# Kernel optimization log

Hardware: AMD Instinct MI355X
Metric: run time of the kernel (lower is better)

The kernel has to match this reference:

```python
import jax, jax.numpy as jnp
import numpy as np

N = 20000
IN_CH = 256
HID = 32
HEADS = 8
OUT_CH = 40
NEG_SLOPE = 0.2


def _gat_layer(x, src, dst, W, a_src, a_dst, b, heads, ch, concat):
    # x: [N, F_in], W: [F_in, heads*ch], a_src/a_dst: [heads, ch], b: [heads*ch] or [ch]
    n = x.shape[0]
    h = (x @ W).reshape(n, heads, ch)                      # [N, H, C]
    alpha_s = jnp.einsum('nhc,hc->nh', h, a_src)           # [N, H]
    alpha_d = jnp.einsum('nhc,hc->nh', h, a_dst)           # [N, H]
    e = jax.nn.leaky_relu(alpha_s[src] + alpha_d[dst], NEG_SLOPE)  # [E, H]
    # segment softmax over edges sharing the same destination node
    m = jax.ops.segment_max(e, dst, num_segments=n)        # [N, H]
    ex = jnp.exp(e - m[dst])                               # [E, H]
    denom = jax.ops.segment_sum(ex, dst, num_segments=n)   # [N, H]
    alpha = ex / (denom[dst] + 1e-16)                      # [E, H]
    out = jax.ops.segment_sum(h[src] * alpha[:, :, None], dst, num_segments=n)  # [N, H, C]
    out = out.reshape(n, heads * ch) if concat else out.mean(axis=1)
    return out + b


def setup_inputs() -> dict:
    key = jax.random.key(0)
    ks = jax.random.split(key, 12)
    x = jax.random.normal(ks[0], (N, IN_CH), dtype=jnp.float32)
    edge_index = jax.random.randint(ks[1], (2, 320000), 0, N, dtype=jnp.int64)
    s1 = 1.0 / np.sqrt(IN_CH)
    s2 = 1.0 / np.sqrt(HEADS * HID)
    W1 = jax.random.uniform(ks[2], (IN_CH, HEADS * HID), jnp.float32, -s1, s1)
    a1_src = jax.random.uniform(ks[3], (HEADS, HID), jnp.float32, -s2, s2)
    a1_dst = jax.random.uniform(ks[4], (HEADS, HID), jnp.float32, -s2, s2)
    b1 = jnp.zeros((HEADS * HID,), jnp.float32)
    W2 = jax.random.uniform(ks[5], (HEADS * HID, OUT_CH), jnp.float32, -s2, s2)
    so = 1.0 / np.sqrt(OUT_CH)
    a2_src = jax.random.uniform(ks[6], (1, OUT_CH), jnp.float32, -so, so)
    a2_dst = jax.random.uniform(ks[7], (1, OUT_CH), jnp.float32, -so, so)
    b2 = jnp.zeros((OUT_CH,), jnp.float32)
    return {"x": x, "edge_index": edge_index, "W1": W1, "a1_src": a1_src,
            "a1_dst": a1_dst, "b1": b1, "W2": W2, "a2_src": a2_src,
            "a2_dst": a2_dst, "b2": b2}


def reference(x, edge_index, W1, a1_src, a1_dst, b1, W2, a2_src, a2_dst, b2):
    n = x.shape[0]
    loop = jnp.arange(n, dtype=edge_index.dtype)
    src = jnp.concatenate([edge_index[0], loop])  # PyG adds self-loops by default
    dst = jnp.concatenate([edge_index[1], loop])
    # dropout layers are identity in eval mode
    h = _gat_layer(x, src, dst, W1, a1_src, a1_dst, b1, HEADS, HID, concat=True)
    h = jax.nn.elu(h)
    out = _gat_layer(h, src, dst, W2, a2_src, a2_dst, b2, 1, OUT_CH, concat=False)
    return jax.nn.log_softmax(out, axis=1)
```

## Files before the change

kernel.cpp:

```cpp
#include <hip/hip_runtime.h>
#include <math.h>

#define N_NODES 20000
#define E_RAW   320000
#define E_TOT   (E_RAW + N_NODES)
#define IN_CH   256
#define HEADS   8
#define HID     32
#define HH      (HEADS*HID)
#define OUT_CH  40
#define NC2     48
#define NEG     0.2f

typedef __attribute__((ext_vector_type(8))) short  short8;
typedef __attribute__((ext_vector_type(4))) float  floatx4;

__device__ __forceinline__ unsigned short f2bf(float f) {
    unsigned int u = __float_as_uint(f);
    unsigned int r = (u + 0x7FFFu + ((u >> 16) & 1u)) >> 16;
    return (unsigned short)r;
}
__device__ __forceinline__ float bf2f(unsigned short h) {
    return __uint_as_float(((unsigned int)h) << 16);
}
__device__ __forceinline__ float lexp(float v) {
    v = (v > 0.f) ? v : NEG * v;
    return __expf(v);
}


__global__ void setup_kernel(const float* __restrict__ W1,
                             const float* __restrict__ W2,
                             unsigned short* __restrict__ w1t,
                             unsigned short* __restrict__ w2t,
                             int* __restrict__ deg) {
    int b = blockIdx.x;
    int t = threadIdx.x;
    if (b < 79) {
        int i = b * 256 + t;
        if (i < N_NODES) deg[i] = 0;
    } else if (b < 79 + HH) {
        int c = b - 79;
        w1t[c * IN_CH + t] = f2bf(W1[(size_t)t * HH + c]);
    } else {
        int c = b - 79 - HH;
        w2t[c * HH + t] = (c < OUT_CH) ? f2bf(W2[(size_t)t * OUT_CH + c]) : 0;
    }
}


__global__ void hist_kernel(const int* __restrict__ ei, int* __restrict__ deg,
                            int* __restrict__ pos) {
    int e = blockIdx.x * 256 + threadIdx.x;
    if (e >= E_TOT) return;
    int d = (e < E_RAW) ? ei[E_RAW + e] : (e - E_RAW);
    pos[e] = atomicAdd(&deg[d], 1);
}

__global__ __launch_bounds__(1024) void scan_kernel(const int* __restrict__ deg,
                                                    int* __restrict__ offs) {
    __shared__ int part[1024];
    int t = threadIdx.x;
    const int chunk = 20;
    int begin = t * chunk;
    bool in = (begin < N_NODES);
    int loc[20];
    if (in) {
        #pragma unroll
        for (int v4 = 0; v4 < 5; v4++) {
            int4 v = *reinterpret_cast<const int4*>(&deg[begin + v4 * 4]);
            loc[v4*4+0] = v.x; loc[v4*4+1] = v.y; loc[v4*4+2] = v.z; loc[v4*4+3] = v.w;
        }
    } else {
        #pragma unroll
        for (int i = 0; i < 20; i++) loc[i] = 0;
    }
    int s = 0;
    #pragma unroll
    for (int i = 0; i < 20; i++) s += loc[i];
    part[t] = s;
    __syncthreads();
    for (int off = 1; off < 1024; off <<= 1) {
        int v = (t >= off) ? part[t - off] : 0;
        __syncthreads();
        part[t] += v;
        __syncthreads();
    }
    int run = (t == 0) ? 0 : part[t - 1];
    if (in) {
        #pragma unroll
        for (int i = 0; i < 20; i++) { offs[begin + i] = run; run += loc[i]; }
    }
    if (t == 1023) offs[N_NODES] = part[1023];
}

__global__ void scatter_kernel(const int* __restrict__ ei, const int* __restrict__ offs,
                               const int* __restrict__ pos, int* __restrict__ csr) {
    int e = blockIdx.x * 256 + threadIdx.x;
    if (e >= E_TOT) return;
    int s, d;
    if (e < E_RAW) { s = ei[e]; d = ei[E_RAW + e]; }
    else           { s = e - E_RAW; d = s; }
    csr[offs[d] + pos[e]] = s;
}

#define G1_LDK 72
__global__ __launch_bounds__(256) void gemm1(const float* __restrict__ x,
                                             const unsigned short* __restrict__ w1t,
                                             const float* __restrict__ a1s,
                                             const float* __restrict__ a1d,
                                             unsigned short* __restrict__ h1b,
                                             float* __restrict__ as1,
                                             float* __restrict__ ad1) {
    __shared__ unsigned short As[64 * G1_LDK];
    __shared__ unsigned short Bs[128 * G1_LDK];
    int t = threadIdx.x;
    int wave = t >> 6, lane = t & 63;
    int ln = lane & 15, q = lane >> 4;
    int bm = blockIdx.x >> 1;
    int bn = blockIdx.x & 1;
    int n0 = bm * 64;
    int c0 = bn * 128;

    floatx4 acc[8];
    #pragma unroll
    for (int f = 0; f < 8; f++) acc[f] = (floatx4){0.f, 0.f, 0.f, 0.f};

    int srow = t >> 4, scol = t & 15;

    for (int kc = 0; kc < IN_CH; kc += 64) {
        #pragma unroll
        for (int pp = 0; pp < 4; pp++) {
            int row = srow + pp * 16;
            int n = n0 + row;
            float4 v = (n < N_NODES)
                ? *reinterpret_cast<const float4*>(&x[(size_t)n * IN_CH + kc + scol * 4])
                : make_float4(0.f, 0.f, 0.f, 0.f);
            ushort4 pv;
            pv.x = f2bf(v.x); pv.y = f2bf(v.y); pv.z = f2bf(v.z); pv.w = f2bf(v.w);
            *reinterpret_cast<ushort4*>(&As[row * G1_LDK + scol * 4]) = pv;
        }
        #pragma unroll
        for (int pp = 0; pp < 8; pp++) {
            int row = srow + pp * 16;
            *reinterpret_cast<ushort4*>(&Bs[row * G1_LDK + scol * 4]) =
                *reinterpret_cast<const ushort4*>(&w1t[(size_t)(c0 + row) * IN_CH + kc + scol * 4]);
        }
        __syncthreads();
        #pragma unroll
        for (int ks = 0; ks < 2; ks++) {
            short8 a = *reinterpret_cast<const short8*>(
                &As[(16 * wave + ln) * G1_LDK + ks * 32 + q * 8]);
            #pragma unroll
            for (int f = 0; f < 8; f++) {
                short8 b = *reinterpret_cast<const short8*>(
                    &Bs[(16 * f + ln) * G1_LDK + ks * 32 + q * 8]);
                acc[f] = __builtin_amdgcn_mfma_f32_16x16x32_bf16(a, b, acc[f], 0, 0, 0);
            }
        }
        __syncthreads();
    }

    float Asr[8], Adr[8];
    #pragma unroll
    for (int f = 0; f < 8; f++) {
        Asr[f] = a1s[c0 + 16 * f + ln];
        Adr[f] = a1d[c0 + 16 * f + ln];
    }
    #pragma unroll
    for (int f = 0; f < 8; f++) {
        #pragma unroll
        for (int r = 0; r < 4; r++) {
            int n = n0 + 16 * wave + q * 4 + r;
            if (n < N_NODES)
                h1b[(size_t)n * HH + c0 + 16 * f + ln] = f2bf(acc[f][r]);
        }
    }
    int h0 = c0 >> 5;
    #pragma unroll
    for (int lh = 0; lh < 4; lh++) {
        #pragma unroll
        for (int r = 0; r < 4; r++) {
            float ps = acc[2*lh][r] * Asr[2*lh] + acc[2*lh+1][r] * Asr[2*lh+1];
            float pd = acc[2*lh][r] * Adr[2*lh] + acc[2*lh+1][r] * Adr[2*lh+1];
            ps += __shfl_xor(ps, 1); ps += __shfl_xor(ps, 2);
            ps += __shfl_xor(ps, 4); ps += __shfl_xor(ps, 8);
            pd += __shfl_xor(pd, 1); pd += __shfl_xor(pd, 2);
            pd += __shfl_xor(pd, 4); pd += __shfl_xor(pd, 8);
            int n = n0 + 16 * wave + q * 4 + r;
            if (ln == 0 && n < N_NODES) {
                as1[n * HEADS + h0 + lh] = ps;
                ad1[n * HEADS + h0 + lh] = pd;
            }
        }
    }
}


__global__ __launch_bounds__(256) void aggr1(const unsigned short* __restrict__ h1b,
                                             const float* __restrict__ as1,
                                             const float* __restrict__ ad1,
                                             const float* __restrict__ b1,
                                             const int* __restrict__ offs,
                                             const int* __restrict__ csr,
                                             unsigned short* __restrict__ h2b) {
    int d = blockIdx.x * 4 + (threadIdx.x >> 6);
    int lane = threadIdx.x & 63;
    int h = lane >> 3;
    int c4 = lane * 4;
    int start = offs[d];
    int deg = offs[d + 1] - start;
    float adv = ad1[d * HEADS + h];

    float a0 = 0.f, a1 = 0.f, a2 = 0.f, a3 = 0.f, den = 0.f;
    int jj = 0;
    for (; jj + 8 <= deg; jj += 8) {
        int s[8];
        #pragma unroll
        for (int i = 0; i < 8; i++) s[i] = csr[start + jj + i];
        float e[8];
        #pragma unroll
        for (int i = 0; i < 8; i++) e[i] = as1[s[i] * HEADS + h];
        ushort4 pv[8];
        #pragma unroll
        for (int i = 0; i < 8; i++)
            pv[i] = *reinterpret_cast<const ushort4*>(&h1b[(size_t)s[i] * HH + c4]);
        #pragma unroll
        for (int i = 0; i < 8; i++) {
            float w = lexp(e[i] + adv);
            den += w;
            a0 = fmaf(bf2f(pv[i].x), w, a0);
            a1 = fmaf(bf2f(pv[i].y), w, a1);
            a2 = fmaf(bf2f(pv[i].z), w, a2);
            a3 = fmaf(bf2f(pv[i].w), w, a3);
        }
    }
    for (; jj < deg; jj++) {
        int s = csr[start + jj];
        float w = lexp(as1[s * HEADS + h] + adv);
        den += w;
        ushort4 pv = *reinterpret_cast<const ushort4*>(&h1b[(size_t)s * HH + c4]);
        a0 = fmaf(bf2f(pv.x), w, a0);
        a1 = fmaf(bf2f(pv.y), w, a1);
        a2 = fmaf(bf2f(pv.z), w, a2);
        a3 = fmaf(bf2f(pv.w), w, a3);
    }
    float inv = 1.0f / (den + 1e-16f);
    float4 bv = *reinterpret_cast<const float4*>(&b1[c4]);
    float r0 = a0 * inv + bv.x;
    float r1 = a1 * inv + bv.y;
    float r2 = a2 * inv + bv.z;
    float r3 = a3 * inv + bv.w;
    r0 = (r0 > 0.f) ? r0 : (__expf(r0) - 1.f);
    r1 = (r1 > 0.f) ? r1 : (__expf(r1) - 1.f);
    r2 = (r2 > 0.f) ? r2 : (__expf(r2) - 1.f);
    r3 = (r3 > 0.f) ? r3 : (__expf(r3) - 1.f);
    ushort4 ov;
    ov.x = f2bf(r0); ov.y = f2bf(r1); ov.z = f2bf(r2); ov.w = f2bf(r3);
    *reinterpret_cast<ushort4*>(&h2b[(size_t)d * HH + c4]) = ov;
}

#define G2_LDK 264
__global__ __launch_bounds__(256) void gemm2(const unsigned short* __restrict__ h2b,
                                             const unsigned short* __restrict__ w2t,
                                             const float* __restrict__ a2s,
                                             const float* __restrict__ a2d,
                                             unsigned short* __restrict__ h3b,
                                             float* __restrict__ as2,
                                             float* __restrict__ ad2) {
    __shared__ unsigned short As2[64 * G2_LDK];
    __shared__ unsigned short Bs2[NC2 * G2_LDK];
    int t = threadIdx.x;
    int wave = t >> 6, lane = t & 63;
    int ln = lane & 15, q = lane >> 4;
    int n0 = blockIdx.x * 64;

    {
        int row = t >> 2, seg = t & 3;
        int n = n0 + row;
        #pragma unroll
        for (int i = 0; i < 8; i++) {
            short8 v;
            if (n < N_NODES)
                v = *reinterpret_cast<const short8*>(&h2b[(size_t)n * HH + seg * 64 + i * 8]);
            else
                v = (short8){0,0,0,0,0,0,0,0};
            *reinterpret_cast<short8*>(&As2[row * G2_LDK + seg * 64 + i * 8]) = v;
        }
    }
    for (int u = t; u < NC2 * 32; u += 256) {
        int row = u >> 5;
        int col = (u & 31) * 8;
        *reinterpret_cast<short8*>(&Bs2[row * G2_LDK + col]) =
            *reinterpret_cast<const short8*>(&w2t[(size_t)row * HH + col]);
    }
    __syncthreads();

    floatx4 acc[3];
    #pragma unroll
    for (int f = 0; f < 3; f++) acc[f] = (floatx4){0.f, 0.f, 0.f, 0.f};

    #pragma unroll
    for (int kf = 0; kf < 8; kf++) {
        short8 a = *reinterpret_cast<const short8*>(
            &As2[(16 * wave + ln) * G2_LDK + kf * 32 + q * 8]);
        #pragma unroll
        for (int f = 0; f < 3; f++) {
            short8 b = *reinterpret_cast<const short8*>(
                &Bs2[(16 * f + ln) * G2_LDK + kf * 32 + q * 8]);
            acc[f] = __builtin_amdgcn_mfma_f32_16x16x32_bf16(a, b, acc[f], 0, 0, 0);
        }
    }

    float a2sv[3], a2dv[3];
    #pragma unroll
    for (int f = 0; f < 3; f++) {
        int c = 16 * f + ln;
        a2sv[f] = (c < OUT_CH) ? a2s[c] : 0.f;
        a2dv[f] = (c < OUT_CH) ? a2d[c] : 0.f;
    }
    #pragma unroll
    for (int r = 0; r < 4; r++) {
        int n = n0 + 16 * wave + q * 4 + r;
        float ps = acc[0][r] * a2sv[0] + acc[1][r] * a2sv[1] + acc[2][r] * a2sv[2];
        float pd = acc[0][r] * a2dv[0] + acc[1][r] * a2dv[1] + acc[2][r] * a2dv[2];
        ps += __shfl_xor(ps, 1); ps += __shfl_xor(ps, 2);
        ps += __shfl_xor(ps, 4); ps += __shfl_xor(ps, 8);
        pd += __shfl_xor(pd, 1); pd += __shfl_xor(pd, 2);
        pd += __shfl_xor(pd, 4); pd += __shfl_xor(pd, 8);
        if (n < N_NODES) {
            #pragma unroll
            for (int f = 0; f < 3; f++) {
                int c = 16 * f + ln;
                if (c < OUT_CH)
                    h3b[(size_t)n * OUT_CH + c] = f2bf(acc[f][r]);
            }
            if (ln == 0) { as2[n] = ps; ad2[n] = pd; }
        }
    }
}


__global__ __launch_bounds__(256) void aggr2(const unsigned short* __restrict__ h3b,
                                             const float* __restrict__ as2,
                                             const float* __restrict__ ad2,
                                             const float* __restrict__ b2,
                                             const int* __restrict__ offs,
                                             const int* __restrict__ csr,
                                             float* __restrict__ out) {
    int d = blockIdx.x * 4 + (threadIdx.x >> 6);
    int lane = threadIdx.x & 63;
    int start = offs[d];
    int deg = offs[d + 1] - start;
    float adv = ad2[d];
    bool ok = (lane < OUT_CH);
    int cl = ok ? lane : 0;

    float acc = 0.f, den = 0.f;
    int jj = 0;
    for (; jj + 8 <= deg; jj += 8) {
        int s[8];
        #pragma unroll
        for (int i = 0; i < 8; i++) s[i] = csr[start + jj + i];
        float e[8];
        #pragma unroll
        for (int i = 0; i < 8; i++) e[i] = as2[s[i]];
        unsigned short qv[8];
        #pragma unroll
        for (int i = 0; i < 8; i++) qv[i] = h3b[(size_t)s[i] * OUT_CH + cl];
        #pragma unroll
        for (int i = 0; i < 8; i++) {
            float w = lexp(e[i] + adv);
            den += w;
            acc = fmaf(bf2f(qv[i]), w, acc);
        }
    }
    for (; jj < deg; jj++) {
        int s = csr[start + jj];
        float w = lexp(as2[s] + adv);
        den += w;
        acc = fmaf(bf2f(h3b[(size_t)s * OUT_CH + cl]), w, acc);
    }

    float r = ok ? (acc / (den + 1e-16f) + b2[lane]) : -1e30f;
    float mx = r;
    #pragma unroll
    for (int off = 32; off >= 1; off >>= 1) mx = fmaxf(mx, __shfl_xor(mx, off));
    float ex = ok ? __expf(r - mx) : 0.f;
    float se = ex;
    #pragma unroll
    for (int off = 32; off >= 1; off >>= 1) se += __shfl_xor(se, off);
    if (ok) out[(size_t)d * OUT_CH + lane] = r - mx - __logf(se);
}


extern "C" void kernel_launch(void* const* d_in, const int* in_sizes, int n_in,
                              void* d_out, int out_size, void* d_ws, size_t ws_size,
                              hipStream_t stream) {
    const float* x   = (const float*)d_in[0];
    const int*   ei  = (const int*)  d_in[1];
    const float* W1  = (const float*)d_in[2];
    const float* a1s = (const float*)d_in[3];
    const float* a1d = (const float*)d_in[4];
    const float* b1  = (const float*)d_in[5];
    const float* W2  = (const float*)d_in[6];
    const float* a2s = (const float*)d_in[7];
    const float* a2d = (const float*)d_in[8];
    const float* b2  = (const float*)d_in[9];
    float* out = (float*)d_out;

    char* p = (char*)d_ws;
    auto alloc = [&](size_t bytes) {
        char* r = p;
        p += (bytes + 255) & ~(size_t)255;
        return r;
    };
    unsigned short* h1b = (unsigned short*)alloc((size_t)N_NODES * HH * 2);
    unsigned short* h2b = (unsigned short*)alloc((size_t)N_NODES * HH * 2);
    unsigned short* h3b = (unsigned short*)alloc((size_t)N_NODES * OUT_CH * 2);
    unsigned short* w1t = (unsigned short*)alloc((size_t)IN_CH * HH * 2);
    unsigned short* w2t = (unsigned short*)alloc((size_t)NC2 * HH * 2);
    float* as1  = (float*)alloc((size_t)N_NODES * HEADS * 4);
    float* ad1  = (float*)alloc((size_t)N_NODES * HEADS * 4);
    float* as2v = (float*)alloc((size_t)N_NODES * 4);
    float* ad2v = (float*)alloc((size_t)N_NODES * 4);
    int* deg    = (int*)alloc((size_t)N_NODES * 4);
    int* pos    = (int*)alloc((size_t)E_TOT * 4);
    int* offs   = (int*)alloc((size_t)(N_NODES + 1) * 4);
    int* csr    = (int*)alloc((size_t)E_TOT * 4);

    setup_kernel<<<79 + HH + NC2, 256, 0, stream>>>(W1, W2, w1t, w2t, deg);
    hist_kernel<<<(E_TOT + 255) / 256, 256, 0, stream>>>(ei, deg, pos);
    scan_kernel<<<1, 1024, 0, stream>>>(deg, offs);
    scatter_kernel<<<(E_TOT + 255) / 256, 256, 0, stream>>>(ei, offs, pos, csr);

    gemm1<<<313 * 2, 256, 0, stream>>>(x, w1t, a1s, a1d, h1b, as1, ad1);
    aggr1<<<N_NODES / 4, 256, 0, stream>>>(h1b, as1, ad1, b1, offs, csr, h2b);
    gemm2<<<313, 256, 0, stream>>>(h2b, w2t, a2s, a2d, h3b, as2v, ad2v);
    aggr2<<<N_NODES / 4, 256, 0, stream>>>(h3b, as2v, ad2v, b2, offs, csr, out);
}
```

Before: 179.9 us.

## Fuse histogram into setup, scatter into gemm1, use wave-shuffle scan

```diff
diff --git a/kernel.cpp b/kernel.cpp
--- a/kernel.cpp
+++ b/kernel.cpp
@@ -12,6 +12,9 @@
 #define NC2     48
 #define NEG     0.2f
 
+#define HIST_BLKS ((E_TOT + 255) / 256)
+#define G1_BLKS   313
+
 typedef __attribute__((ext_vector_type(8))) short  short8;
 typedef __attribute__((ext_vector_type(4))) float  floatx4;
 
@@ -29,38 +32,35 @@
 }
 
 
-__global__ void setup_kernel(const float* __restrict__ W1,
-                             const float* __restrict__ W2,
-                             unsigned short* __restrict__ w1t,
-                             unsigned short* __restrict__ w2t,
-                             int* __restrict__ deg) {
+__global__ void setup_hist(const int* __restrict__ ei,
+                           const float* __restrict__ W1,
+                           const float* __restrict__ W2,
+                           unsigned short* __restrict__ w1t,
+                           unsigned short* __restrict__ w2t,
+                           int* __restrict__ deg,
+                           int* __restrict__ pos) {
     int b = blockIdx.x;
     int t = threadIdx.x;
-    if (b < 79) {
-        int i = b * 256 + t;
-        if (i < N_NODES) deg[i] = 0;
-    } else if (b < 79 + HH) {
-        int c = b - 79;
+    if (b < HIST_BLKS) {
+        int e = b * 256 + t;
+        if (e >= E_TOT) return;
+        int d = (e < E_RAW) ? ei[E_RAW + e] : (e - E_RAW);
+        pos[e] = atomicAdd(&deg[d], 1);
+    } else if (b < HIST_BLKS + HH) {
+        int c = b - HIST_BLKS;
         w1t[c * IN_CH + t] = f2bf(W1[(size_t)t * HH + c]);
     } else {
-        int c = b - 79 - HH;
-        w2t[c * HH + t] = (c < OUT_CH) ? f2bf(W2[(size_t)t * OUT_CH + c]) : 0;
-    }
-}
-
-
-__global__ void hist_kernel(const int* __restrict__ ei, int* __restrict__ deg,
-                            int* __restrict__ pos) {
-    int e = blockIdx.x * 256 + threadIdx.x;
-    if (e >= E_TOT) return;
-    int d = (e < E_RAW) ? ei[E_RAW + e] : (e - E_RAW);
-    pos[e] = atomicAdd(&deg[d], 1);
-}
+        int c = b - HIST_BLKS - HH;
+        w2t[c * HH + t] = (c < OUT_CH) ? f2bf(W2[(size_t)t * OUT_CH + c]) : (unsigned short)0;
+    }
+}
+
 
 __global__ __launch_bounds__(1024) void scan_kernel(const int* __restrict__ deg,
                                                     int* __restrict__ offs) {
-    __shared__ int part[1024];
+    __shared__ int wsum[16], wpre[16];
     int t = threadIdx.x;
+    int lane = t & 63, wave = t >> 6;
     const int chunk = 20;
     int begin = t * chunk;
     bool in = (begin < N_NODES);
@@ -78,30 +78,38 @@
     int s = 0;
     #pragma unroll
     for (int i = 0; i < 20; i++) s += loc[i];
-    part[t] = s;
+    int sc = s;
+    #pragma unroll
+    for (int off = 1; off < 64; off <<= 1) {
+        int v = __shfl_up(sc, off);
+        if (lane >= off) sc += v;
+    }
+    if (lane == 63) wsum[wave] = sc;
     __syncthreads();
-    for (int off = 1; off < 1024; off <<= 1) {
-        int v = (t >= off) ? part[t - off] : 0;
-        __syncthreads();
-        part[t] += v;
-        __syncthreads();
-    }
-    int run = (t == 0) ? 0 : part[t - 1];
+    if (t < 16) {
+        int v = wsum[t];
+        int p = v;
+        #pragma unroll
+        for (int off = 1; off < 16; off <<= 1) {
+            int u = __shfl_up(p, off);
+            if (t >= off) p += u;
+        }
+        wpre[t] = p - v;
+    }
+    __syncthreads();
+    int run = wpre[wave] + sc - s;
     if (in) {
         #pragma unroll
-        for (int i = 0; i < 20; i++) { offs[begin + i] = run; run += loc[i]; }
-    }
-    if (t == 1023) offs[N_NODES] = part[1023];
-}
-
-__global__ void scatter_kernel(const int* __restrict__ ei, const int* __restrict__ offs,
-                               const int* __restrict__ pos, int* __restrict__ csr) {
-    int e = blockIdx.x * 256 + threadIdx.x;
-    if (e >= E_TOT) return;
-    int s, d;
-    if (e < E_RAW) { s = ei[e]; d = ei[E_RAW + e]; }
-    else           { s = e - E_RAW; d = s; }
-    csr[offs[d] + pos[e]] = s;
+        for (int v4 = 0; v4 < 5; v4++) {
+            int4 o;
+            o.x = run; run += loc[v4*4+0];
+            o.y = run; run += loc[v4*4+1];
+            o.z = run; run += loc[v4*4+2];
+            o.w = run; run += loc[v4*4+3];
+            *reinterpret_cast<int4*>(&offs[begin + v4 * 4]) = o;
+        }
+    }
+    if (t == 0) offs[N_NODES] = E_TOT;
 }
 
 #define G1_LDK 72
@@ -111,20 +119,33 @@
                                              const float* __restrict__ a1d,
                                              unsigned short* __restrict__ h1b,
                                              float* __restrict__ as1,
-                                             float* __restrict__ ad1) {
+                                             float* __restrict__ ad1,
+                                             const int* __restrict__ ei,
+                                             const int* __restrict__ offs,
+                                             const int* __restrict__ pos,
+                                             int* __restrict__ csr) {
     __shared__ unsigned short As[64 * G1_LDK];
-    __shared__ unsigned short Bs[128 * G1_LDK];
+    __shared__ unsigned short Bs[256 * G1_LDK];
     int t = threadIdx.x;
+
+    if (blockIdx.x >= G1_BLKS) {
+        int e = (blockIdx.x - G1_BLKS) * 256 + t;
+        if (e < E_TOT) {
+            int s, d;
+            if (e < E_RAW) { s = ei[e]; d = ei[E_RAW + e]; }
+            else           { s = e - E_RAW; d = s; }
+            csr[offs[d] + pos[e]] = s;
+        }
+        return;
+    }
+
     int wave = t >> 6, lane = t & 63;
     int ln = lane & 15, q = lane >> 4;
-    int bm = blockIdx.x >> 1;
-    int bn = blockIdx.x & 1;
-    int n0 = bm * 64;
-    int c0 = bn * 128;
-
-    floatx4 acc[8];
-    #pragma unroll
-    for (int f = 0; f < 8; f++) acc[f] = (floatx4){0.f, 0.f, 0.f, 0.f};
+    int n0 = blockIdx.x * 64;
+
+    floatx4 acc[16];
+    #pragma unroll
+    for (int f = 0; f < 16; f++) acc[f] = (floatx4){0.f, 0.f, 0.f, 0.f};
 
     int srow = t >> 4, scol = t & 15;
 
@@ -141,10 +162,10 @@
             *reinterpret_cast<ushort4*>(&As[row * G1_LDK + scol * 4]) = pv;
         }
         #pragma unroll
-        for (int pp = 0; pp < 8; pp++) {
+        for (int pp = 0; pp < 16; pp++) {
             int row = srow + pp * 16;
             *reinterpret_cast<ushort4*>(&Bs[row * G1_LDK + scol * 4]) =
-                *reinterpret_cast<const ushort4*>(&w1t[(size_t)(c0 + row) * IN_CH + kc + scol * 4]);
+                *reinterpret_cast<const ushort4*>(&w1t[(size_t)row * IN_CH + kc + scol * 4]);
         }
         __syncthreads();
         #pragma unroll
@@ -152,7 +173,7 @@
             short8 a = *reinterpret_cast<const short8*>(
                 &As[(16 * wave + ln) * G1_LDK + ks * 32 + q * 8]);
             #pragma unroll
-            for (int f = 0; f < 8; f++) {
+            for (int f = 0; f < 16; f++) {
                 short8 b = *reinterpret_cast<const short8*>(
                     &Bs[(16 * f + ln) * G1_LDK + ks * 32 + q * 8]);
                 acc[f] = __builtin_amdgcn_mfma_f32_16x16x32_bf16(a, b, acc[f], 0, 0, 0);
@@ -161,24 +182,23 @@
         __syncthreads();
     }
 
-    float Asr[8], Adr[8];
-    #pragma unroll
-    for (int f = 0; f < 8; f++) {
-        Asr[f] = a1s[c0 + 16 * f + ln];
-        Adr[f] = a1d[c0 + 16 * f + ln];
-    }
-    #pragma unroll
-    for (int f = 0; f < 8; f++) {
+    float Asr[16], Adr[16];
+    #pragma unroll
+    for (int f = 0; f < 16; f++) {
+        Asr[f] = a1s[16 * f + ln];
+        Adr[f] = a1d[16 * f + ln];
+    }
+    #pragma unroll
+    for (int f = 0; f < 16; f++) {
         #pragma unroll
         for (int r = 0; r < 4; r++) {
             int n = n0 + 16 * wave + q * 4 + r;
             if (n < N_NODES)
-                h1b[(size_t)n * HH + c0 + 16 * f + ln] = f2bf(acc[f][r]);
-        }
-    }
-    int h0 = c0 >> 5;
-    #pragma unroll
-    for (int lh = 0; lh < 4; lh++) {
+                h1b[(size_t)n * HH + 16 * f + ln] = f2bf(acc[f][r]);
+        }
+    }
+    #pragma unroll
+    for (int lh = 0; lh < 8; lh++) {
         #pragma unroll
         for (int r = 0; r < 4; r++) {
             float ps = acc[2*lh][r] * Asr[2*lh] + acc[2*lh+1][r] * Asr[2*lh+1];
@@ -189,8 +209,8 @@
             pd += __shfl_xor(pd, 4); pd += __shfl_xor(pd, 8);
             int n = n0 + 16 * wave + q * 4 + r;
             if (ln == 0 && n < N_NODES) {
-                as1[n * HEADS + h0 + lh] = ps;
-                ad1[n * HEADS + h0 + lh] = pd;
+                as1[n * HEADS + lh] = ps;
+                ad1[n * HEADS + lh] = pd;
             }
         }
     }
@@ -429,12 +449,11 @@
     int* offs   = (int*)alloc((size_t)(N_NODES + 1) * 4);
     int* csr    = (int*)alloc((size_t)E_TOT * 4);
 
-    setup_kernel<<<79 + HH + NC2, 256, 0, stream>>>(W1, W2, w1t, w2t, deg);
-    hist_kernel<<<(E_TOT + 255) / 256, 256, 0, stream>>>(ei, deg, pos);
+    hipMemsetAsync(deg, 0, (size_t)N_NODES * sizeof(int), stream);
+    setup_hist<<<HIST_BLKS + HH + NC2, 256, 0, stream>>>(ei, W1, W2, w1t, w2t, deg, pos);
     scan_kernel<<<1, 1024, 0, stream>>>(deg, offs);
-    scatter_kernel<<<(E_TOT + 255) / 256, 256, 0, stream>>>(ei, offs, pos, csr);
-
-    gemm1<<<313 * 2, 256, 0, stream>>>(x, w1t, a1s, a1d, h1b, as1, ad1);
+    gemm1<<<G1_BLKS + HIST_BLKS, 256, 0, stream>>>(x, w1t, a1s, a1d, h1b, as1, ad1,
+                                                   ei, offs, pos, csr);
     aggr1<<<N_NODES / 4, 256, 0, stream>>>(h1b, as1, ad1, b1, offs, csr, h2b);
     gemm2<<<313, 256, 0, stream>>>(h2b, w2t, a2s, a2d, h3b, as2v, ad2v);
     aggr2<<<N_NODES / 4, 256, 0, stream>>>(h3b, as2v, ad2v, b2, offs, csr, out);
```

Result: slower. 192.7 us (+7.1%).
